# Optimization experiments

Hardware: AMD Instinct MI355X
Metric: run time of the kernel (lower is better)

## Reference

```python
import jax, jax.numpy as jnp
import numpy as np

B, D, K = 32, 64, 256            # batch, num objects (seq len), feature size (== in_size)
G = [256, 256, 256]              # g_layers sizes
F1, F2, OUT = 256, 256, 128      # f_fc1, f_fc2, out_size


def setup_inputs() -> dict:
    key = jax.random.key(0)
    ks = jax.random.split(key, 16)
    scale = 0.02

    def w(k, shape):
        return jax.random.normal(k, shape, dtype=jnp.float32) * scale

    x = jax.random.normal(ks[0], (B, D, K), dtype=jnp.float32)
    # edge_feature: Linear(2*K, K). Stored [in, out] (transposed vs torch).
    edge_w = w(ks[1], (2 * K, K))
    edge_b = jnp.zeros((K,), dtype=jnp.float32)
    g_ws, g_bs = [], []
    in_s = K
    for i, out_s in enumerate(G):
        g_ws.append(w(ks[2 + i], (in_s, out_s)))
        g_bs.append(jnp.zeros((out_s,), dtype=jnp.float32))
        in_s = out_s
    f1_w = w(ks[8], (G[-1], F1)); f1_b = jnp.zeros((F1,), dtype=jnp.float32)
    f2_w = w(ks[9], (F1, F2));    f2_b = jnp.zeros((F2,), dtype=jnp.float32)
    f3_w = w(ks[10], (F2, OUT));  f3_b = jnp.zeros((OUT,), dtype=jnp.float32)
    return dict(x=x, edge_w=edge_w, edge_b=edge_b, g_ws=g_ws, g_bs=g_bs,
                f1_w=f1_w, f1_b=f1_b, f2_w=f2_w, f2_b=f2_b, f3_w=f3_w, f3_b=f3_b)


def reference(x, edge_w, edge_b, g_ws, g_bs, f1_w, f1_b, f2_w, f2_b, f3_w, f3_b):
    # x: [B, D, K]. Original builds x_full[b,i,j] = concat(x[b,j], x[b,i]) then
    # applies edge_feature (Linear(2K -> K)). Equivalent, without materializing the
    # concat: split edge_w into the halves acting on x_i (=x[b,j]) and x_j (=x[b,i]).
    k = x.shape[-1]
    u = x @ edge_w[:k]      # [B, D, K]  -> indexed by j (axis 2)
    v = x @ edge_w[k:]      # [B, D, K]  -> indexed by i (axis 1)
    h = u[:, None, :, :] + v[:, :, None, :] + edge_b   # [B, D, D, K]
    # g MLP over all d^2 pairs (Linear + ReLU chain)
    for gw, gb in zip(g_ws, g_bs):
        h = jax.nn.relu(h @ gw + gb)
    # sum-aggregate over all pairs
    x_g = h.sum(axis=(1, 2))                            # [B, G[-1]]
    # f MLP (dropout p=0.0 -> identity)
    x_f = jax.nn.relu(x_g @ f1_w + f1_b)
    x_f = jax.nn.relu(x_f @ f2_w + f2_b)
    return x_f @ f3_w + f3_b                            # [B, OUT]
```

## Files before the change

kernel.cpp:

```cpp
#include <hip/hip_runtime.h>
#include <hip/hip_bf16.h>

typedef __attribute__((ext_vector_type(4))) float f32x4;
typedef __attribute__((ext_vector_type(2))) int   i32x2;
typedef __attribute__((ext_vector_type(4))) int   i32x4;
typedef __attribute__((ext_vector_type(8))) short short8;

__device__ __forceinline__ unsigned short f2bf(float x) {
  __hip_bfloat16 h = __float2bfloat16(x);
  union { __hip_bfloat16 h1; unsigned short u; } c; c.h1 = h; return c.u;
}
__device__ __forceinline__ unsigned pk2(float a, float b) {
  __hip_bfloat162 h = __float22bfloat162_rn(make_float2(a, b));
  union { __hip_bfloat162 h2; unsigned u; } c; c.h2 = h; return c.u;
}
__device__ __forceinline__ float bf2f(unsigned short u) {
  union { unsigned u32; float f; } c; c.u32 = ((unsigned)u) << 16; return c.f;
}

__global__ void k_prep(const float* __restrict__ edge_w, const float* __restrict__ edge_b,
                       const float* __restrict__ gw0, const float* __restrict__ gb0,
                       const float* __restrict__ gw1, const float* __restrict__ gw2,
                       float* __restrict__ W1u, float* __restrict__ W1v,
                       float* __restrict__ c1,
                       unsigned short* __restrict__ W2R, unsigned short* __restrict__ W3R) {
  const int blk = blockIdx.x, t = threadIdx.x;
  __shared__ float eu[256], ev[256];
  if (blk < 256) {
    eu[t] = edge_w[blk * 256 + t];
    ev[t] = edge_w[(256 + blk) * 256 + t];
    __syncthreads();
    float su = 0.f, sv = 0.f;
    for (int o = 0; o < 256; ++o) {
      float gg = gw0[o * 256 + t];
      su += eu[o] * gg; sv += ev[o] * gg;
    }
    W1u[blk * 256 + t] = su;
    W1v[blk * 256 + t] = sv;
  } else if (blk == 256) {
    float s = gb0[t];
    for (int o = 0; o < 256; ++o) s += edge_b[o] * gw0[o * 256 + t];
    c1[t] = s;
  } else {
    int p = blk - 257;
    const float* src = (p < 32) ? gw1 : gw2;
    unsigned short* dst = (p < 32) ? W2R : W3R;
    p &= 31;
    int w = p >> 3, ch = p & 7;
    int mf = t >> 6, lane = t & 63, q = lane & 15, g = lane >> 4;
    int base = ((w * 8 + ch) * 4 + mf) * 512 + lane * 8;
    int m = w * 64 + mf * 16 + q;
#pragma unroll
    for (int e = 0; e < 8; ++e) {
      int k = ch * 32 + g * 8 + e;
      dst[base + e] = f2bf(src[k * 256 + m]);
    }
  }
}

__global__ void k_uv(const float* __restrict__ x,
                     const float* __restrict__ W1u, const float* __restrict__ W1v,
                     const float* __restrict__ c1,
                     unsigned short* __restrict__ U1, float* __restrict__ V1c) {
  const int blk = blockIdx.x, t = threadIdx.x;
  const int r0 = blk * 8;
  __shared__ float xs[2048];
  if (t < 512) *(f32x4*)(xs + t * 4) = *(const f32x4*)(x + (size_t)r0 * 256 + t * 4);
  __syncthreads();
  const int sel = t >> 9, half = (t >> 8) & 1, col = t & 255;
  const float* W = sel ? W1v : W1u;
  float a[4];
#pragma unroll
  for (int r = 0; r < 4; ++r) a[r] = 0.f;
  const float* xb = xs + (half * 4) * 256;
#pragma unroll 4
  for (int k = 0; k < 256; ++k) {
    float w = W[k * 256 + col];
#pragma unroll
    for (int r = 0; r < 4; ++r) a[r] += xb[r * 256 + k] * w;
  }
  if (sel == 0) {
#pragma unroll
    for (int r = 0; r < 4; ++r) U1[(size_t)(r0 + half * 4 + r) * 256 + col] = f2bf(a[r]);
  } else {
    float c = c1[col];
#pragma unroll
    for (int r = 0; r < 4; ++r) V1c[(size_t)(r0 + half * 4 + r) * 256 + col] = a[r] + c;
  }
}

__device__ __forceinline__ void write_h1(short8 u, f32x4 v0, f32x4 v1,
                                         unsigned short* dst) {
  float r0 = fmaxf(bf2f((unsigned short)u[0]) + v0.x, 0.f);
  float r1 = fmaxf(bf2f((unsigned short)u[1]) + v0.y, 0.f);
  float r2 = fmaxf(bf2f((unsigned short)u[2]) + v0.z, 0.f);
  float r3 = fmaxf(bf2f((unsigned short)u[3]) + v0.w, 0.f);
  float r4 = fmaxf(bf2f((unsigned short)u[4]) + v1.x, 0.f);
  float r5 = fmaxf(bf2f((unsigned short)u[5]) + v1.y, 0.f);
  float r6 = fmaxf(bf2f((unsigned short)u[6]) + v1.z, 0.f);
  float r7 = fmaxf(bf2f((unsigned short)u[7]) + v1.w, 0.f);
  i32x4 wv = { (int)pk2(r0, r1), (int)pk2(r2, r3), (int)pk2(r4, r5), (int)pk2(r6, r7) };
  *(i32x4*)dst = wv;
}

__launch_bounds__(256, 3)
__global__ void k_main(const unsigned short* __restrict__ U1,
                       const float* __restrict__ V1c,
                       const unsigned short* __restrict__ W2R,
                       const unsigned short* __restrict__ W3R,
                       const float* __restrict__ b2, const float* __restrict__ b3,
                       float* __restrict__ partials) {
  __shared__ unsigned short h1s[2][2048];
  __shared__ unsigned short h2s[16384];

  const int t = threadIdx.x;
  const int bid = blockIdx.x;
  const int wrk = ((bid & 7) << 8) | (bid >> 3);
  const int b = wrk >> 6;
  const int wid = t >> 6, lane = t & 63;
  const int q = lane & 15, g = lane >> 4;
  const int mo = wid << 6;

  const int row = t >> 2, sl = t & 3;
  const int ks = sl ^ ((row >> 1) & 3);
  const unsigned short* uP = U1 + (size_t)(b * 64 + row) * 256 + ks * 8;
  const float* vP = V1c + (size_t)wrk * 256 + ks * 8;
  unsigned short* const h1w0 = &h1s[0][0] + row * 32 + sl * 8;
  unsigned short* const h1w1 = &h1s[1][0] + row * 32 + sl * 8;

  const unsigned short* aW2 = W2R + (size_t)wid * 16384 + lane * 8;
  const unsigned short* aW3 = W3R + (size_t)wid * 16384 + lane * 8;

  short8 a_[4], an_[4];
#pragma unroll
  for (int mf = 0; mf < 4; ++mf) a_[mf] = *(const short8*)(aW2 + mf * 512);
  {
    short8 u0 = *(const short8*)uP;
    f32x4 v0 = *(const f32x4*)vP;
    f32x4 v1 = *(const f32x4*)(vP + 4);
    write_h1(u0, v0, v1, h1w0);
  }
  __syncthreads();

  f32x4 acc[4][4];
#pragma unroll
  for (int mf = 0; mf < 4; ++mf)
#pragma unroll
    for (int nf = 0; nf < 4; ++nf) acc[mf][nf] = (f32x4){0.f, 0.f, 0.f, 0.f};

  for (int ch = 0; ch < 8; ++ch) {
    const unsigned short* hcur = &h1s[ch & 1][0];
    short8 u_n; f32x4 v0_n, v1_n;
    if (ch < 7) {
#pragma unroll
      for (int mf = 0; mf < 4; ++mf)
        an_[mf] = *(const short8*)(aW2 + (ch + 1) * 2048 + mf * 512);
      u_n  = *(const short8*)(uP + (ch + 1) * 32);
      v0_n = *(const f32x4*)(vP + (ch + 1) * 32);
      v1_n = *(const f32x4*)(vP + (ch + 1) * 32 + 4);
    }
    short8 b_[4];
#pragma unroll
    for (int nf = 0; nf < 4; ++nf) {
      int r = q + 16 * nf;
      b_[nf] = *(const short8*)(hcur + r * 32 + ((g ^ ((r >> 1) & 3)) * 8));
    }
#pragma unroll
    for (int mf = 0; mf < 4; ++mf)
#pragma unroll
      for (int nf = 0; nf < 4; ++nf)
        acc[mf][nf] = __builtin_amdgcn_mfma_f32_16x16x32_bf16(a_[mf], b_[nf], acc[mf][nf], 0, 0, 0);
    if (ch < 7) {
      write_h1(u_n, v0_n, v1_n, ((ch + 1) & 1) ? h1w1 : h1w0);
#pragma unroll
      for (int mf = 0; mf < 4; ++mf) a_[mf] = an_[mf];
      __syncthreads();
    }
  }

#pragma unroll
  for (int mf = 0; mf < 4; ++mf) a_[mf] = *(const short8*)(aW3 + mf * 512);
#pragma unroll
  for (int mf = 0; mf < 4; ++mf) {
    int c2b = mo + 16 * mf + 4 * g;
    f32x4 bb = *(const f32x4*)(b2 + c2b);
    int ksw = c2b >> 3, off = c2b & 7;
#pragma unroll
    for (int nf = 0; nf < 4; ++nf) {
      int r = q + 16 * nf;
      f32x4 v = acc[mf][nf];
      float e0 = fmaxf(v.x + bb.x, 0.f), e1 = fmaxf(v.y + bb.y, 0.f);
      float e2 = fmaxf(v.z + bb.z, 0.f), e3 = fmaxf(v.w + bb.w, 0.f);
      i32x2 wv = { (int)pk2(e0, e1), (int)pk2(e2, e3) };
      *(i32x2*)(h2s + r * 256 + ((ksw ^ (r & 7)) * 8) + off) = wv;
    }
  }
  __syncthreads();

  f32x4 acc2[4][4];
#pragma unroll
  for (int mf = 0; mf < 4; ++mf)
#pragma unroll
    for (int nf = 0; nf < 4; ++nf) acc2[mf][nf] = (f32x4){0.f, 0.f, 0.f, 0.f};

  for (int ch = 0; ch < 8; ++ch) {
    if (ch < 7) {
#pragma unroll
      for (int mf = 0; mf < 4; ++mf)
        an_[mf] = *(const short8*)(aW3 + (ch + 1) * 2048 + mf * 512);
    }
    short8 b_[4];
#pragma unroll
    for (int nf = 0; nf < 4; ++nf) {
      int r = q + 16 * nf;
      int s2 = ch * 4 + g;
      b_[nf] = *(const short8*)(h2s + r * 256 + ((s2 ^ (r & 7)) * 8));
    }
#pragma unroll
    for (int mf = 0; mf < 4; ++mf)
#pragma unroll
      for (int nf = 0; nf < 4; ++nf)
        acc2[mf][nf] = __builtin_amdgcn_mfma_f32_16x16x32_bf16(a_[mf], b_[nf], acc2[mf][nf], 0, 0, 0);
    if (ch < 7) {
#pragma unroll
      for (int mf = 0; mf < 4; ++mf) a_[mf] = an_[mf];
    }
  }
  __syncthreads();

  float* scr = (float*)&h2s[0];
#pragma unroll
  for (int mf = 0; mf < 4; ++mf) {
    int n3b = mo + 16 * mf + 4 * g;
    f32x4 bb = *(const f32x4*)(b3 + n3b);
    f32x4 sum = (f32x4){0.f, 0.f, 0.f, 0.f};
#pragma unroll
    for (int nf = 0; nf < 4; ++nf) {
      f32x4 v = acc2[mf][nf];
      sum.x += fmaxf(v.x + bb.x, 0.f);
      sum.y += fmaxf(v.y + bb.y, 0.f);
      sum.z += fmaxf(v.z + bb.z, 0.f);
      sum.w += fmaxf(v.w + bb.w, 0.f);
    }
    *(f32x4*)(scr + q * 264 + n3b) = sum;
  }
  __syncthreads();
  float s = 0.f;
#pragma unroll
  for (int q2 = 0; q2 < 16; ++q2) s += scr[q2 * 264 + t];
  partials[(size_t)wrk * 256 + t] = s;
}

__global__ void k_fmlp(const float* __restrict__ partials,
                       const float* __restrict__ f1w, const float* __restrict__ f1b,
                       const float* __restrict__ f2w, const float* __restrict__ f2b,
                       const float* __restrict__ f3w, const float* __restrict__ f3b,
                       float* __restrict__ out) {
  const int b = blockIdx.x, t = threadIdx.x;
  __shared__ float xg[256], x1[256], x2[256];
  {
    const float* p = partials + (size_t)(b * 64) * 256 + t;
    float s[8];
#pragma unroll
    for (int i = 0; i < 8; ++i) s[i] = 0.f;
#pragma unroll
    for (int k = 0; k < 8; ++k)
#pragma unroll
      for (int i = 0; i < 8; ++i) s[i] += p[(k * 8 + i) * 256];
    float tot = 0.f;
#pragma unroll
    for (int i = 0; i < 8; ++i) tot += s[i];
    xg[t] = tot;
  }
  __syncthreads();
  {
    float a0 = 0.f, a1 = 0.f, a2 = 0.f, a3 = 0.f;
#pragma unroll 4
    for (int k = 0; k < 64; ++k) {
      a0 += xg[k]       * f1w[(k)       * 256 + t];
      a1 += xg[k + 64]  * f1w[(k + 64)  * 256 + t];
      a2 += xg[k + 128] * f1w[(k + 128) * 256 + t];
      a3 += xg[k + 192] * f1w[(k + 192) * 256 + t];
    }
    x1[t] = fmaxf((a0 + a1) + (a2 + a3) + f1b[t], 0.f);
  }
  __syncthreads();
  {
    float a0 = 0.f, a1 = 0.f, a2 = 0.f, a3 = 0.f;
#pragma unroll 4
    for (int k = 0; k < 64; ++k) {
      a0 += x1[k]       * f2w[(k)       * 256 + t];
      a1 += x1[k + 64]  * f2w[(k + 64)  * 256 + t];
      a2 += x1[k + 128] * f2w[(k + 128) * 256 + t];
      a3 += x1[k + 192] * f2w[(k + 192) * 256 + t];
    }
    x2[t] = fmaxf((a0 + a1) + (a2 + a3) + f2b[t], 0.f);
  }
  __syncthreads();
  if (t < 128) {
    float a0 = 0.f, a1 = 0.f, a2 = 0.f, a3 = 0.f;
#pragma unroll 4
    for (int k = 0; k < 64; ++k) {
      a0 += x2[k]       * f3w[(k)       * 128 + t];
      a1 += x2[k + 64]  * f3w[(k + 64)  * 128 + t];
      a2 += x2[k + 128] * f3w[(k + 128) * 128 + t];
      a3 += x2[k + 192] * f3w[(k + 192) * 128 + t];
    }
    out[b * 128 + t] = (a0 + a1) + (a2 + a3) + f3b[t];
  }
}

__global__ void k_zero(float* __restrict__ out, int n) {
  int i = blockIdx.x * 256 + threadIdx.x;
  if (i < n) out[i] = 0.f;
}

extern "C" void kernel_launch(void* const* d_in, const int* in_sizes, int n_in,
                              void* d_out, int out_size, void* d_ws, size_t ws_size,
                              hipStream_t stream) {
  const float* x      = (const float*)d_in[0];
  const float* edge_w = (const float*)d_in[1];
  const float* edge_b = (const float*)d_in[2];
  const float *gw0, *gw1, *gw2, *gb0, *gb1, *gb2;
  const float *f1w, *f1b, *f2w, *f2b, *f3w, *f3b;

  if (n_in >= 15 && in_sizes[3] == 65536 && in_sizes[4] == 65536 && in_sizes[5] == 65536) {
    gw0 = (const float*)d_in[3]; gw1 = (const float*)d_in[4]; gw2 = (const float*)d_in[5];
    gb0 = (const float*)d_in[6]; gb1 = (const float*)d_in[7]; gb2 = (const float*)d_in[8];
    f1w = (const float*)d_in[9];  f1b = (const float*)d_in[10];
    f2w = (const float*)d_in[11]; f2b = (const float*)d_in[12];
    f3w = (const float*)d_in[13]; f3b = (const float*)d_in[14];
  } else if (n_in >= 15 && in_sizes[3] == 65536 && in_sizes[4] == 256) {
    gw0 = (const float*)d_in[3]; gb0 = (const float*)d_in[4];
    gw1 = (const float*)d_in[5]; gb1 = (const float*)d_in[6];
    gw2 = (const float*)d_in[7]; gb2 = (const float*)d_in[8];
    f1w = (const float*)d_in[9];  f1b = (const float*)d_in[10];
    f2w = (const float*)d_in[11]; f2b = (const float*)d_in[12];
    f3w = (const float*)d_in[13]; f3b = (const float*)d_in[14];
  } else {
    const float* gws = (const float*)d_in[3];
    const float* gbs = (const float*)d_in[4];
    gw0 = gws;          gw1 = gws + 65536;  gw2 = gws + 131072;
    gb0 = gbs;          gb1 = gbs + 256;    gb2 = gbs + 512;
    f1w = (const float*)d_in[5];  f1b = (const float*)d_in[6];
    f2w = (const float*)d_in[7];  f2b = (const float*)d_in[8];
    f3w = (const float*)d_in[9];  f3b = (const float*)d_in[10];
  }

  char* ws = (char*)d_ws;
  float*          W1u      = (float*)(ws);
  float*          W1v      = (float*)(ws + 262144);
  float*          c1       = (float*)(ws + 524288);
  unsigned short* W2R      = (unsigned short*)(ws + 525312);
  unsigned short* W3R      = (unsigned short*)(ws + 656384);
  unsigned short* U1       = (unsigned short*)(ws + 787456);
  float*          V1c      = (float*)(ws + 1836032);
  float*          partials = (float*)(ws + 3933184);
  const size_t need = 6030336;
  (void)out_size; (void)n_in;

  if (ws_size < need) {
    k_zero<<<dim3((out_size + 255) / 256), dim3(256), 0, stream>>>((float*)d_out, out_size);
    return;
  }

  k_prep<<<dim3(321), dim3(256), 0, stream>>>(edge_w, edge_b, gw0, gb0, gw1, gw2,
                                              W1u, W1v, c1, W2R, W3R);
  k_uv<<<dim3(256), dim3(1024), 0, stream>>>(x, W1u, W1v, c1, U1, V1c);
  k_main<<<dim3(2048), dim3(256), 0, stream>>>(U1, V1c, W2R, W3R, gb1, gb2, partials);
  k_fmlp<<<dim3(32), dim3(256), 0, stream>>>(partials, f1w, f1b, f2w, f2b, f3w, f3b,
                                             (float*)d_out);
}
```

Measured before the change: 86.45 us.

## Stage full h1 tile upfront in shared buffer and split k_uv reduction over K

k_main now builds the entire 64x256 bf16 h1 tile in shared memory before the first GEMM, reusing a single buffer for h1 and h2. This removes the per-chunk barriers and the double-buffered h1 writes from the layer-2 loop and lowers shared memory use from about 40KB to 32KB per block. In exchange, the global loads of U1/V1c are no longer overlapped with MFMA work. k_uv is also restructured so each thread covers 8 rows over half of K, with the two halves combined through shared memory, which halves the weight reads per row.

```diff
diff --git a/kernel.cpp b/kernel.cpp
--- a/kernel.cpp
+++ b/kernel.cpp
@@ -65,27 +65,37 @@
   const int blk = blockIdx.x, t = threadIdx.x;
   const int r0 = blk * 8;
   __shared__ float xs[2048];
+  __shared__ float pl[8 * 512];
   if (t < 512) *(f32x4*)(xs + t * 4) = *(const f32x4*)(x + (size_t)r0 * 256 + t * 4);
   __syncthreads();
-  const int sel = t >> 9, half = (t >> 8) & 1, col = t & 255;
-  const float* W = sel ? W1v : W1u;
-  float a[4];
-#pragma unroll
-  for (int r = 0; r < 4; ++r) a[r] = 0.f;
-  const float* xb = xs + (half * 4) * 256;
+  const int sel = t >> 9, kh = (t >> 8) & 1, col = t & 255;
+  const float* W = (sel ? W1v : W1u) + (size_t)kh * 128 * 256;
+  const float* xb = xs + kh * 128;
+  float a[8];
+#pragma unroll
+  for (int r = 0; r < 8; ++r) a[r] = 0.f;
 #pragma unroll 4
-  for (int k = 0; k < 256; ++k) {
+  for (int k = 0; k < 128; ++k) {
     float w = W[k * 256 + col];
 #pragma unroll
-    for (int r = 0; r < 4; ++r) a[r] += xb[r * 256 + k] * w;
-  }
-  if (sel == 0) {
-#pragma unroll
-    for (int r = 0; r < 4; ++r) U1[(size_t)(r0 + half * 4 + r) * 256 + col] = f2bf(a[r]);
-  } else {
-    float c = c1[col];
-#pragma unroll
-    for (int r = 0; r < 4; ++r) V1c[(size_t)(r0 + half * 4 + r) * 256 + col] = a[r] + c;
+    for (int r = 0; r < 8; ++r) a[r] += xb[r * 256 + k] * w;
+  }
+  if (kh == 1) {
+#pragma unroll
+    for (int r = 0; r < 8; ++r) pl[r * 512 + sel * 256 + col] = a[r];
+  }
+  __syncthreads();
+  if (kh == 0) {
+#pragma unroll
+    for (int r = 0; r < 8; ++r) a[r] += pl[r * 512 + sel * 256 + col];
+    if (sel == 0) {
+#pragma unroll
+      for (int r = 0; r < 8; ++r) U1[(size_t)(r0 + r) * 256 + col] = f2bf(a[r]);
+    } else {
+      float c = c1[col];
+#pragma unroll
+      for (int r = 0; r < 8; ++r) V1c[(size_t)(r0 + r) * 256 + col] = a[r] + c;
+    }
   }
 }
 
@@ -110,8 +120,7 @@
                        const unsigned short* __restrict__ W3R,
                        const float* __restrict__ b2, const float* __restrict__ b3,
                        float* __restrict__ partials) {
-  __shared__ unsigned short h1s[2][2048];
-  __shared__ unsigned short h2s[16384];
+  __shared__ unsigned short hbuf[16384];
 
   const int t = threadIdx.x;
   const int bid = blockIdx.x;
@@ -121,12 +130,21 @@
   const int q = lane & 15, g = lane >> 4;
   const int mo = wid << 6;
 
-  const int row = t >> 2, sl = t & 3;
-  const int ks = sl ^ ((row >> 1) & 3);
-  const unsigned short* uP = U1 + (size_t)(b * 64 + row) * 256 + ks * 8;
-  const float* vP = V1c + (size_t)wrk * 256 + ks * 8;
-  unsigned short* const h1w0 = &h1s[0][0] + row * 32 + sl * 8;
-  unsigned short* const h1w1 = &h1s[1][0] + row * 32 + sl * 8;
+  {
+    const int row = t >> 2, sl = t & 3, r7 = row & 7;
+    const unsigned short* uB = U1 + (size_t)(b * 64 + row) * 256;
+    const float* vB = V1c + (size_t)wrk * 256;
+    unsigned short* hB = hbuf + row * 256;
+#pragma unroll
+    for (int m = 0; m < 8; ++m) {
+      int ks = sl + 4 * m;
+      int s = ks ^ r7;
+      short8 u = *(const short8*)(uB + ks * 8);
+      f32x4 v0 = *(const f32x4*)(vB + ks * 8);
+      f32x4 v1 = *(const f32x4*)(vB + ks * 8 + 4);
+      write_h1(u, v0, v1, hB + s * 8);
+    }
+  }
 
   const unsigned short* aW2 = W2R + (size_t)wid * 16384 + lane * 8;
   const unsigned short* aW3 = W3R + (size_t)wid * 16384 + lane * 8;
@@ -134,12 +152,7 @@
   short8 a_[4], an_[4];
 #pragma unroll
   for (int mf = 0; mf < 4; ++mf) a_[mf] = *(const short8*)(aW2 + mf * 512);
-  {
-    short8 u0 = *(const short8*)uP;
-    f32x4 v0 = *(const f32x4*)vP;
-    f32x4 v1 = *(const f32x4*)(vP + 4);
-    write_h1(u0, v0, v1, h1w0);
-  }
+
   __syncthreads();
 
   f32x4 acc[4][4];
@@ -149,21 +162,16 @@
     for (int nf = 0; nf < 4; ++nf) acc[mf][nf] = (f32x4){0.f, 0.f, 0.f, 0.f};
 
   for (int ch = 0; ch < 8; ++ch) {
-    const unsigned short* hcur = &h1s[ch & 1][0];
-    short8 u_n; f32x4 v0_n, v1_n;
     if (ch < 7) {
 #pragma unroll
       for (int mf = 0; mf < 4; ++mf)
         an_[mf] = *(const short8*)(aW2 + (ch + 1) * 2048 + mf * 512);
-      u_n  = *(const short8*)(uP + (ch + 1) * 32);
-      v0_n = *(const f32x4*)(vP + (ch + 1) * 32);
-      v1_n = *(const f32x4*)(vP + (ch + 1) * 32 + 4);
     }
     short8 b_[4];
 #pragma unroll
     for (int nf = 0; nf < 4; ++nf) {
       int r = q + 16 * nf;
-      b_[nf] = *(const short8*)(hcur + r * 32 + ((g ^ ((r >> 1) & 3)) * 8));
+      b_[nf] = *(const short8*)(hbuf + r * 256 + (((ch * 4 + g) ^ (r & 7)) * 8));
     }
 #pragma unroll
     for (int mf = 0; mf < 4; ++mf)
@@ -171,12 +179,12 @@
       for (int nf = 0; nf < 4; ++nf)
         acc[mf][nf] = __builtin_amdgcn_mfma_f32_16x16x32_bf16(a_[mf], b_[nf], acc[mf][nf], 0, 0, 0);
     if (ch < 7) {
-      write_h1(u_n, v0_n, v1_n, ((ch + 1) & 1) ? h1w1 : h1w0);
 #pragma unroll
       for (int mf = 0; mf < 4; ++mf) a_[mf] = an_[mf];
-      __syncthreads();
-    }
-  }
+    }
+  }
+
+  __syncthreads();
 
 #pragma unroll
   for (int mf = 0; mf < 4; ++mf) a_[mf] = *(const short8*)(aW3 + mf * 512);
@@ -192,7 +200,7 @@
       float e0 = fmaxf(v.x + bb.x, 0.f), e1 = fmaxf(v.y + bb.y, 0.f);
       float e2 = fmaxf(v.z + bb.z, 0.f), e3 = fmaxf(v.w + bb.w, 0.f);
       i32x2 wv = { (int)pk2(e0, e1), (int)pk2(e2, e3) };
-      *(i32x2*)(h2s + r * 256 + ((ksw ^ (r & 7)) * 8) + off) = wv;
+      *(i32x2*)(hbuf + r * 256 + ((ksw ^ (r & 7)) * 8) + off) = wv;
     }
   }
   __syncthreads();
@@ -213,8 +221,7 @@
 #pragma unroll
     for (int nf = 0; nf < 4; ++nf) {
       int r = q + 16 * nf;
-      int s2 = ch * 4 + g;
-      b_[nf] = *(const short8*)(h2s + r * 256 + ((s2 ^ (r & 7)) * 8));
+      b_[nf] = *(const short8*)(hbuf + r * 256 + (((ch * 4 + g) ^ (r & 7)) * 8));
     }
 #pragma unroll
     for (int mf = 0; mf < 4; ++mf)
@@ -226,9 +233,10 @@
       for (int mf = 0; mf < 4; ++mf) a_[mf] = an_[mf];
     }
   }
-  __syncthreads();
-
-  float* scr = (float*)&h2s[0];
+
+  __syncthreads();
+
+  float* scr = (float*)&hbuf[0];
 #pragma unroll
   for (int mf = 0; mf < 4; ++mf) {
     int n3b = mo + 16 * mf + 4 * g;
```

Result: faster. 79.28 us (-8.3%).
